# Kernel optimization log

Hardware: AMD Instinct MI355X
Metric: run time of the kernel (lower is better)

The kernel has to match this reference:

```python
import jax, jax.numpy as jnp
import numpy as np

EPS = 1e-3  # keras LayerNormalization default epsilon


def layer_norm(x, g, b):
    mu = jnp.mean(x, axis=-1, keepdims=True)
    var = jnp.mean(jnp.square(x - mu), axis=-1, keepdims=True)
    return g * (x - mu) / jnp.sqrt(var + EPS) + b


def setup_inputs() -> dict:
    key = jax.random.key(0)
    ks = jax.random.split(key, 16)
    B, S, E, H, F = 2, 4096, 512, 8, 2048
    s_e = 1.0 / np.sqrt(E)
    s_f = 1.0 / np.sqrt(F)
    inp = {
        "x": jax.random.normal(ks[0], (B, S, E), dtype=jnp.float32),
        "WQ": jax.random.normal(ks[1], (E, E), dtype=jnp.float32) * s_e,
        "bQ": jnp.zeros((E,), jnp.float32),
        "WK": jax.random.normal(ks[2], (E, E), dtype=jnp.float32) * s_e,
        "bK": jnp.zeros((E,), jnp.float32),
        "WV": jax.random.normal(ks[3], (E, E), dtype=jnp.float32) * s_e,
        "bV": jnp.zeros((E,), jnp.float32),
        "WO": jax.random.normal(ks[4], (E, E), dtype=jnp.float32) * s_e,
        "bO": jnp.zeros((E,), jnp.float32),
        "W1": jax.random.normal(ks[5], (E, F), dtype=jnp.float32) * s_e,
        "b1": jnp.zeros((F,), jnp.float32),
        "W2": jax.random.normal(ks[6], (F, E), dtype=jnp.float32) * s_f,
        "b2": jnp.zeros((E,), jnp.float32),
        "g1": jnp.ones((E,), jnp.float32),
        "beta1": jnp.zeros((E,), jnp.float32),
        "g2": jnp.ones((E,), jnp.float32),
        "beta2": jnp.zeros((E,), jnp.float32),
        "num_head": 8,
    }
    return inp


def reference(x, WQ, bQ, WK, bK, WV, bV, WO, bO, W1, b1, W2, b2,
              g1, beta1, g2, beta2, num_head):
    B, S, E = x.shape
    H = num_head
    d = E // H
    scale = jnp.sqrt(jnp.asarray(d, jnp.float32))

    q = (x @ WQ + bQ).reshape(B, S, H, d).transpose(0, 2, 1, 3)  # [B,H,S,d]
    k = (x @ WK + bK).reshape(B, S, H, d).transpose(0, 2, 1, 3)
    v = (x @ WV + bV).reshape(B, S, H, d).transpose(0, 2, 1, 3)

    score = jnp.einsum('bhqd,bhkd->bhqk', q, k) / scale  # O(S^2) materialized, as in source
    attn = jax.nn.softmax(score, axis=-1)
    zs = jnp.einsum('bhqk,bhkd->bhqd', attn, v)  # [B,H,S,d]

    # Faithful to source bug: reshape [B,H,S,d] -> [B,S,E] WITHOUT transposing back
    zs = zs.reshape(B, S, E)
    zs = zs @ WO + bO

    z = layer_norm(zs + x, g1, beta1)
    r = jax.nn.relu(z @ W1 + b1) @ W2 + b2
    r = layer_norm(r + z, g2, beta2)
    return r
```

## Files before the change

kernel.cpp:

```cpp
#include <hip/hip_runtime.h>
#include <hip/hip_bf16.h>

typedef unsigned short u16;
typedef __attribute__((ext_vector_type(8))) short bf16x8;
typedef __attribute__((ext_vector_type(4))) float f32x4;
typedef __attribute__((ext_vector_type(16))) float f32x16;

static constexpr int BB = 2;
static constexpr int SS = 4096;
static constexpr int EE = 512;
static constexpr int HH = 8;
static constexpr int DD = 64;
static constexpr int FF = 2048;
static constexpr int NR = BB * SS;
static constexpr int QS = 3 * EE;

#define QSCALE 0.18033688011112042f

__device__ __forceinline__ u16 f2bf(float f) {
  union { float f; unsigned u; } v; v.f = f;
  unsigned r = v.u + 0x7FFFu + ((v.u >> 16) & 1u);
  return (u16)(r >> 16);
}
__device__ __forceinline__ unsigned pack2(float a, float b) {
  return (unsigned)f2bf(a) | ((unsigned)f2bf(b) << 16);
}
__device__ __forceinline__ float bf2f_lo(unsigned u) {
  union { unsigned u; float f; } v; v.u = u << 16; return v.f;
}
__device__ __forceinline__ float bf2f_hi(unsigned u) {
  union { unsigned u; float f; } v; v.u = u & 0xffff0000u; return v.f;
}
__device__ __forceinline__ unsigned cvtpk(float lo, float hi) {
  unsigned r;
  asm("v_cvt_pk_bf16_f32 %0, %1, %2" : "=v"(r) : "v"(lo), "v"(hi));
  return r;
}
__device__ __forceinline__ void perm32swap(unsigned& a, unsigned& b) {
  asm("v_permlane32_swap_b32 %0, %1" : "+v"(a), "+v"(b));
}
__device__ __forceinline__ void gload_lds16(const u16* g, u16* l) {
  __builtin_amdgcn_global_load_lds(
      (const __attribute__((address_space(1))) unsigned*)g,
      (__attribute__((address_space(3))) unsigned*)l, 16, 0, 0);
}

struct TrJob { const float* W; u16* Wt; int K, N, k0, n0; };

__device__ __forceinline__ void transp_tile(const float* W, u16* Wt, int K,
                                            int N, int k0, int n0, int t) {
  __shared__ float T[64][65];
  const int tn = t & 63, tk = t >> 6;
#pragma unroll
  for (int i = 0; i < 16; ++i) {
    int kk = tk * 16 + i;
    T[kk][tn] = W[(size_t)(k0 + kk) * N + n0 + tn];
  }
  __syncthreads();
#pragma unroll
  for (int i = 0; i < 16; ++i) {
    int nn = tk * 16 + i;
    Wt[(size_t)(n0 + nn) * K + k0 + tn] = f2bf(T[tn][nn]);
  }
}

__global__ __launch_bounds__(256) void prep_all(
    const float* __restrict__ x, u16* __restrict__ xb,
    const float* __restrict__ WQ, const float* __restrict__ WK,
    const float* __restrict__ WV, const float* __restrict__ WO,
    const float* __restrict__ W1, const float* __restrict__ W2,
    u16* __restrict__ Wqkv_t, u16* __restrict__ WO_t, u16* __restrict__ W1_t,
    u16* __restrict__ W2_t, const float* __restrict__ bQ,
    const float* __restrict__ bK, const float* __restrict__ bV,
    float* __restrict__ bqkv) {
  const int bx = blockIdx.x;
  const int t = threadIdx.x;
  if (bx < 2048) {
    int i = (bx * 256 + t) * 8;
    float4 a = *(const float4*)(x + i);
    float4 b = *(const float4*)(x + i + 4);
    uint4 u;
    u.x = pack2(a.x, a.y); u.y = pack2(a.z, a.w);
    u.z = pack2(b.x, b.y); u.w = pack2(b.z, b.w);
    *(uint4*)(xb + i) = u;
    return;
  }
  int idx = bx - 2048;
  if (idx < 768) {
    TrJob j;
    if (idx < 256) {
      const float* srcs[4] = {WQ, WK, WV, WO};
      u16* dsts[4] = {Wqkv_t, Wqkv_t + 512 * 512, Wqkv_t + 1024 * 512, WO_t};
      int w = idx >> 6, l = idx & 63;
      j = {srcs[w], dsts[w], 512, 512, (l & 7) * 64, (l >> 3) * 64};
    } else if (idx < 512) {
      int l = idx - 256;
      j = {W1, W1_t, 512, 2048, (l & 7) * 64, (l >> 3) * 64};
    } else {
      int l = idx - 512;
      j = {W2, W2_t, 2048, 512, (l & 31) * 64, (l >> 5) * 64};
    }
    transp_tile(j.W, j.Wt, j.K, j.N, j.k0, j.n0, t);
    return;
  }
  for (int i = t; i < QS; i += 256)
    bqkv[i] = i < 512 ? bQ[i] : (i < 1024 ? bK[i - 512] : bV[i - 1024]);
}

__global__ __launch_bounds__(256) void transp_v(const u16* __restrict__ qkvb,
                                                u16* __restrict__ vt) {
  __shared__ u16 T[64][72];
  const int s0 = blockIdx.x * 64, c0 = blockIdx.y * 64, b = blockIdx.z;
  const int t = threadIdx.x;
#pragma unroll
  for (int i = 0; i < 2; ++i) {
    int idx = t + i * 256;
    int row = idx >> 3, c8 = idx & 7;
    *(uint4*)(&T[row][c8 * 8]) = *(const uint4*)(
        &qkvb[((size_t)b * SS + s0 + row) * QS + 1024 + c0 + c8 * 8]);
  }
  __syncthreads();
#pragma unroll
  for (int i = 0; i < 2; ++i) {
    int idx = t + i * 256;
    int c = idx >> 3, s8 = idx & 7;
    u16 tmp[8];
#pragma unroll
    for (int j = 0; j < 8; ++j) tmp[j] = T[s8 * 8 + j][c];
    *(uint4*)(&vt[((size_t)b * EE + c0 + c) * SS + s0 + s8 * 8]) =
        *(uint4*)tmp;
  }
}

template <int RELU, int OUT_BF16, int SCALEQ = 0>
__global__ __launch_bounds__(256) void gemm128(
    const u16* __restrict__ A, const u16* __restrict__ Bt,
    const float* __restrict__ bias, void* __restrict__ Cout,
    int M, int N, int K) {
  __shared__ __align__(16) u16 As[128 * 64];
  __shared__ __align__(16) u16 Bs[128 * 64];
  const int t = threadIdx.x;
  const int lane = t & 63, wid = t >> 6;
  const int lm = lane & 15, lg = lane >> 4;
  const int bm = blockIdx.x * 128, bn = blockIdx.y * 128;
  const int wr = (wid >> 1) * 64, wc = (wid & 1) * 64;
  const int sr = lane >> 3;
  const int scb = (lane & 7) ^ sr;

  f32x4 acc[4][4];
#pragma unroll
  for (int i = 0; i < 4; ++i)
#pragma unroll
    for (int j = 0; j < 4; ++j) acc[i][j] = (f32x4){0.f, 0.f, 0.f, 0.f};

  for (int kb = 0; kb < K; kb += 64) {
    __syncthreads();
#pragma unroll
    for (int i = 0; i < 4; ++i) {
      int rr = wid * 32 + i * 8 + sr;
      gload_lds16(A + (size_t)(bm + rr) * K + kb + scb * 8,
                  &As[(wid * 32 + i * 8) * 64]);
      gload_lds16(Bt + (size_t)(bn + rr) * K + kb + scb * 8,
                  &Bs[(wid * 32 + i * 8) * 64]);
    }
    __syncthreads();

#pragma unroll
    for (int c = 0; c < 2; ++c) {
      bf16x8 af[4], bfr[4];
#pragma unroll
      for (int i = 0; i < 4; ++i) {
        int ar = wr + i * 16 + lm;
        af[i] = *(const bf16x8*)(&As[ar * 64 + (((c * 4 + lg) ^ (ar & 7)) << 3)]);
        int br = wc + i * 16 + lm;
        bfr[i] = *(const bf16x8*)(&Bs[br * 64 + (((c * 4 + lg) ^ (br & 7)) << 3)]);
      }
#pragma unroll
      for (int i = 0; i < 4; ++i)
#pragma unroll
        for (int j = 0; j < 4; ++j)
          acc[i][j] = __builtin_amdgcn_mfma_f32_16x16x32_bf16(
              af[i], bfr[j], acc[i][j], 0, 0, 0);
    }
  }

  float bi[4];
#pragma unroll
  for (int j = 0; j < 4; ++j) bi[j] = bias[bn + wc + j * 16 + lm];

#pragma unroll
  for (int i = 0; i < 4; ++i) {
#pragma unroll
    for (int j = 0; j < 4; ++j) {
      int col = bn + wc + j * 16 + lm;
#pragma unroll
      for (int r = 0; r < 4; ++r) {
        int row = bm + wr + i * 16 + lg * 4 + r;
        float vv = acc[i][j][r] + bi[j];
        if (RELU) vv = fmaxf(vv, 0.f);
        if (SCALEQ && col < 512) vv *= QSCALE;
        if (OUT_BF16)
          ((u16*)Cout)[(size_t)row * N + col] = f2bf(vv);
        else
          ((float*)Cout)[(size_t)row * N + col] = vv;
      }
    }
  }
}

template <int RELU, int OUT_BF16, int SCALEQ = 0>
__global__ __launch_bounds__(256) void gemm64(
    const u16* __restrict__ A, const u16* __restrict__ Bt,
    const float* __restrict__ bias, void* __restrict__ Cout,
    int M, int N, int K) {
  __shared__ __align__(16) u16 As[2][64 * 64];
  __shared__ __align__(16) u16 Bs[2][64 * 64];
  const int t = threadIdx.x;
  const int lane = t & 63, wid = t >> 6;
  const int lm = lane & 15, lg = lane >> 4;
  const int bm = blockIdx.x * 64, bn = blockIdx.y * 64;
  const int wr = (wid >> 1) * 32, wc = (wid & 1) * 32;
  const int sr = lane >> 3;
  const int scb = (lane & 7) ^ sr;

  f32x4 acc[2][2];
#pragma unroll
  for (int i = 0; i < 2; ++i)
#pragma unroll
    for (int j = 0; j < 2; ++j) acc[i][j] = (f32x4){0.f, 0.f, 0.f, 0.f};

  auto stage = [&](int kb, int buf) {
#pragma unroll
    for (int i = 0; i < 2; ++i) {
      int r8 = wid * 16 + i * 8;
      gload_lds16(A + (size_t)(bm + r8 + sr) * K + kb + scb * 8,
                  &As[buf][r8 * 64]);
      gload_lds16(Bt + (size_t)(bn + r8 + sr) * K + kb + scb * 8,
                  &Bs[buf][r8 * 64]);
    }
  };

  stage(0, 0);
  const int nsteps = K >> 6;
  for (int s = 0; s < nsteps; ++s) {
    const int cur = s & 1;
    if (s + 1 < nsteps) {
      stage((s + 1) << 6, cur ^ 1);
      asm volatile("s_waitcnt vmcnt(4)" ::: "memory");
    } else {
      asm volatile("s_waitcnt vmcnt(0)" ::: "memory");
    }
    __builtin_amdgcn_sched_barrier(0);
    __builtin_amdgcn_s_barrier();

#pragma unroll
    for (int c = 0; c < 2; ++c) {
      bf16x8 af[2], bfr[2];
#pragma unroll
      for (int i = 0; i < 2; ++i) {
        int ar = wr + i * 16 + lm;
        af[i] = *(const bf16x8*)(
            &As[cur][ar * 64 + (((c * 4 + lg) ^ (ar & 7)) << 3)]);
        int br = wc + i * 16 + lm;
        bfr[i] = *(const bf16x8*)(
            &Bs[cur][br * 64 + (((c * 4 + lg) ^ (br & 7)) << 3)]);
      }
#pragma unroll
      for (int i = 0; i < 2; ++i)
#pragma unroll
        for (int j = 0; j < 2; ++j)
          acc[i][j] = __builtin_amdgcn_mfma_f32_16x16x32_bf16(
              af[i], bfr[j], acc[i][j], 0, 0, 0);
    }

    asm volatile("s_waitcnt lgkmcnt(0)" ::: "memory");
    __builtin_amdgcn_s_barrier();
  }

  float bi[2];
#pragma unroll
  for (int j = 0; j < 2; ++j) bi[j] = bias[bn + wc + j * 16 + lm];

#pragma unroll
  for (int i = 0; i < 2; ++i) {
#pragma unroll
    for (int j = 0; j < 2; ++j) {
      int col = bn + wc + j * 16 + lm;
#pragma unroll
      for (int r = 0; r < 4; ++r) {
        int row = bm + wr + i * 16 + lg * 4 + r;
        float vv = acc[i][j][r] + bi[j];
        if (RELU) vv = fmaxf(vv, 0.f);
        if (SCALEQ && col < 512) vv *= QSCALE;
        if (OUT_BF16)
          ((u16*)Cout)[(size_t)row * N + col] = f2bf(vv);
        else
          ((float*)Cout)[(size_t)row * N + col] = vv;
      }
    }
  }
}

__global__ __launch_bounds__(128, 4) void attn_split(
    const u16* __restrict__ qkv, const u16* __restrict__ vt,
    u16* __restrict__ po, float* __restrict__ pl) {
  __shared__ __align__(16) u16 K_lds[2][32 * 64];
  __shared__ __align__(16) u16 V_lds[2][64 * 32];

  const int bh = blockIdx.x;
  const int qblock = blockIdx.y;
  const int half = blockIdx.z;
  po += (size_t)half * (9u << 19);
  pl += (size_t)half * (1u << 18);
  const int b = bh >> 3, h = bh & 7;
  const int t = threadIdx.x;
  const int lane = t & 63, wid = t >> 6;
  const int q32 = lane & 31, hi = lane >> 5;
  const int qs7 = q32 & 7;
  const int vswz = (q32 & 3) ^ ((q32 >> 2) & 3);
  const size_t bS = (size_t)b * SS;
  const int koff0 = half * 2048;
  const u16* kp = qkv + 512;
  const u16* vrow = vt + ((size_t)b * EE + h * DD) * SS;
  const int qbase = qblock * 64 + wid * 32;

  bf16x8 qf[4];
  {
    const u16* qrow = qkv + (bS + qbase + q32) * QS + h * DD + hi * 8;
#pragma unroll
    for (int c = 0; c < 4; ++c) qf[c] = *(const bf16x8*)(qrow + c * 16);
  }
  bf16x8 onesf;
#pragma unroll
  for (int i = 0; i < 8; ++i) onesf[i] = (short)0x3F80;

  const int sr = lane >> 3;
  const int scb = (lane & 7) ^ sr;
  const int vr = lane >> 2;
  const int vcb = (lane & 3) ^ (vr & 3) ^ ((vr >> 2) & 3);

  f32x16 o0, o1, ol, z16;
#pragma unroll
  for (int i = 0; i < 16; ++i) {
    o0[i] = 0.f; o1[i] = 0.f; ol[i] = 0.f; z16[i] = 0.f;
  }

  auto stage = [&](int kt, int bufi) {
#pragma unroll
    for (int i = 0; i < 2; ++i) {
      int rb = wid * 16 + i * 8;
      gload_lds16(
          kp + (bS + koff0 + kt * 32 + rb + sr) * QS + h * DD + scb * 8,
          &K_lds[bufi][rb * 64]);
    }
#pragma unroll
    for (int i = 0; i < 2; ++i) {
      int rb = wid * 32 + i * 16;
      gload_lds16(vrow + (size_t)(rb + vr) * SS + koff0 + kt * 32 + vcb * 8,
                  &V_lds[bufi][rb * 32]);
    }
  };

  stage(0, 0);

  constexpr int NT = 2048 / 32;
  for (int kt = 0; kt < NT; ++kt) {
    const int cur = kt & 1;
    if (kt + 1 < NT) {
      stage(kt + 1, cur ^ 1);
      asm volatile("s_waitcnt vmcnt(4)" ::: "memory");
    } else {
      asm volatile("s_waitcnt vmcnt(0)" ::: "memory");
    }
    __builtin_amdgcn_sched_barrier(0);
    __builtin_amdgcn_s_barrier();

    f32x16 s;
    __builtin_amdgcn_s_setprio(1);
    {
      bf16x8 kf = *(const bf16x8*)(
          &K_lds[cur][q32 * 64 + ((hi ^ qs7) << 3)]);
      s = __builtin_amdgcn_mfma_f32_32x32x16_bf16(kf, qf[0], z16, 0, 0, 0);
    }
#pragma unroll
    for (int c = 1; c < 4; ++c) {
      bf16x8 kf = *(const bf16x8*)(
          &K_lds[cur][q32 * 64 + (((2 * c + hi) ^ qs7) << 3)]);
      s = __builtin_amdgcn_mfma_f32_32x32x16_bf16(kf, qf[c], s, 0, 0, 0);
    }
    __builtin_amdgcn_s_setprio(0);
    float p[16];
#pragma unroll
    for (int r = 0; r < 16; ++r) p[r] = __builtin_amdgcn_exp2f(s[r]);

    __builtin_amdgcn_s_setprio(1);
#pragma unroll
    for (int kc = 0; kc < 2; ++kc) {
      const int rA = kc * 8, rB = rA + 4;
      unsigned wA0 = cvtpk(p[rA + 0], p[rA + 1]);
      unsigned wA1 = cvtpk(p[rA + 2], p[rA + 3]);
      unsigned wB0 = cvtpk(p[rB + 0], p[rB + 1]);
      unsigned wB1 = cvtpk(p[rB + 2], p[rB + 3]);
      perm32swap(wA0, wB0);
      perm32swap(wA1, wB1);
      union { unsigned u[4]; bf16x8 v; } pf;
      pf.u[0] = wA0; pf.u[1] = wA1; pf.u[2] = wB0; pf.u[3] = wB1;
      bf16x8 vf0 = *(const bf16x8*)(
          &V_lds[cur][q32 * 32 + (((2 * kc + hi) ^ vswz) << 3)]);
      bf16x8 vf1 = *(const bf16x8*)(
          &V_lds[cur][(32 + q32) * 32 + (((2 * kc + hi) ^ vswz) << 3)]);
      o0 = __builtin_amdgcn_mfma_f32_32x32x16_bf16(pf.v, vf0, o0, 0, 0, 0);
      o1 = __builtin_amdgcn_mfma_f32_32x32x16_bf16(pf.v, vf1, o1, 0, 0, 0);
      ol = __builtin_amdgcn_mfma_f32_32x32x16_bf16(pf.v, onesf, ol, 0, 0, 0);
    }
    __builtin_amdgcn_s_setprio(0);

    asm volatile("s_waitcnt lgkmcnt(0)" ::: "memory");
    __builtin_amdgcn_s_barrier();
  }

  const size_t rowbase = (size_t)bh * 4096 + qbase;
#pragma unroll
  for (int reg = 0; reg < 16; ++reg) {
    int q = (reg & 3) + 8 * (reg >> 2) + 4 * hi;
    if (q32 == q) pl[rowbase + q] = ol[reg];
    u16* dst = po + (rowbase + q) * 64;
    dst[q32] = f2bf(o0[reg]);
    dst[32 + q32] = f2bf(o1[reg]);
  }
}

__global__ __launch_bounds__(256) void attn_combine(
    const u16* __restrict__ po0, const u16* __restrict__ po1,
    const float* __restrict__ pl0, const float* __restrict__ pl1,
    u16* __restrict__ zs) {
  const int row = blockIdx.x * 32 + (threadIdx.x >> 3);
  const int dblk = (threadIdx.x & 7) * 8;
  const int bh = row >> 12, s = row & 4095;
  const int b = bh >> 3, h = bh & 7;
  const float inv = 1.f / (pl0[row] + pl1[row]);
  uint4 a = *(const uint4*)(po0 + (size_t)row * 64 + dblk);
  uint4 c = *(const uint4*)(po1 + (size_t)row * 64 + dblk);
  uint4 r;
  r.x = pack2((bf2f_lo(a.x) + bf2f_lo(c.x)) * inv,
              (bf2f_hi(a.x) + bf2f_hi(c.x)) * inv);
  r.y = pack2((bf2f_lo(a.y) + bf2f_lo(c.y)) * inv,
              (bf2f_hi(a.y) + bf2f_hi(c.y)) * inv);
  r.z = pack2((bf2f_lo(a.z) + bf2f_lo(c.z)) * inv,
              (bf2f_hi(a.z) + bf2f_hi(c.z)) * inv);
  r.w = pack2((bf2f_lo(a.w) + bf2f_lo(c.w)) * inv,
              (bf2f_hi(a.w) + bf2f_hi(c.w)) * inv);
  u16* dst = zs + ((size_t)b * SS + h * 512 + (s >> 3)) * EE + (s & 7) * 64;
  *(uint4*)(dst + dblk) = r;
}

template <int WF32>
__global__ __launch_bounds__(128) void add_ln_b(
    const u16* __restrict__ a, const u16* __restrict__ xres,
    const float* __restrict__ g, const float* __restrict__ beta,
    u16* __restrict__ outb, float* __restrict__ outf) {
  const int row = blockIdx.x;
  const int tid = threadIdx.x;
  uint2 av = *(const uint2*)(a + (size_t)row * EE + tid * 4);
  uint2 xv = *(const uint2*)(xres + (size_t)row * EE + tid * 4);
  float vx = bf2f_lo(av.x) + bf2f_lo(xv.x);
  float vy = bf2f_hi(av.x) + bf2f_hi(xv.x);
  float vz = bf2f_lo(av.y) + bf2f_lo(xv.y);
  float vw = bf2f_hi(av.y) + bf2f_hi(xv.y);
  float sum = vx + vy + vz + vw;
  float sq = vx * vx + vy * vy + vz * vz + vw * vw;
#pragma unroll
  for (int off = 1; off < 64; off <<= 1) {
    sum += __shfl_xor(sum, off);
    sq += __shfl_xor(sq, off);
  }
  __shared__ float s0[2], s1[2];
  int w = tid >> 6;
  if ((tid & 63) == 0) { s0[w] = sum; s1[w] = sq; }
  __syncthreads();
  sum = s0[0] + s0[1];
  sq = s1[0] + s1[1];
  float mu = sum * (1.0f / EE);
  float var = sq * (1.0f / EE) - mu * mu;
  float r = rsqrtf(var + 1e-3f);
  int c = tid * 4;
  float4 gv = *(const float4*)(g + c);
  float4 bv = *(const float4*)(beta + c);
  float o0 = gv.x * (vx - mu) * r + bv.x;
  float o1 = gv.y * (vy - mu) * r + bv.y;
  float o2 = gv.z * (vz - mu) * r + bv.z;
  float o3 = gv.w * (vw - mu) * r + bv.w;
  if (WF32) {
    float4 ov = {o0, o1, o2, o3};
    *(float4*)(outf + (size_t)row * EE + c) = ov;
  } else {
    uint2 u;
    u.x = pack2(o0, o1);
    u.y = pack2(o2, o3);
    *(uint2*)(outb + (size_t)row * EE + c) = u;
  }
}

extern "C" void kernel_launch(void* const* d_in, const int* in_sizes, int n_in,
                              void* d_out, int out_size, void* d_ws,
                              size_t ws_size, hipStream_t stream) {
  const float* x = (const float*)d_in[0];
  const float* WQ = (const float*)d_in[1];
  const float* bQ = (const float*)d_in[2];
  const float* WK = (const float*)d_in[3];
  const float* bK = (const float*)d_in[4];
  const float* WV = (const float*)d_in[5];
  const float* bV = (const float*)d_in[6];
  const float* WO = (const float*)d_in[7];
  const float* bO = (const float*)d_in[8];
  const float* W1 = (const float*)d_in[9];
  const float* b1 = (const float*)d_in[10];
  const float* W2 = (const float*)d_in[11];
  const float* b2 = (const float*)d_in[12];
  const float* g1 = (const float*)d_in[13];
  const float* be1 = (const float*)d_in[14];
  const float* g2 = (const float*)d_in[15];
  const float* be2 = (const float*)d_in[16];
  float* out = (float*)d_out;

  const size_t MB = 1u << 20;
  char* w = (char*)d_ws;
  u16* Wqkv_t = (u16*)(w + 0);
  u16* WO_t   = (u16*)(w + 2 * MB);
  u16* W1_t   = (u16*)(w + 3 * MB);
  u16* W2_t   = (u16*)(w + 5 * MB);
  float* bqkv = (float*)(w + 7 * MB);
  u16* qkvb = (u16*)(w + 8 * MB);
  u16* zsb  = (u16*)(w + 32 * MB);
  u16* po0  = (u16*)(w + 40 * MB);
  u16* po1  = (u16*)(w + 49 * MB);
  float* pl0 = (float*)(w + 58 * MB);
  float* pl1 = (float*)(w + 59 * MB);
  u16* zs2b = (u16*)(w + 40 * MB);
  u16* f2b  = (u16*)(w + 49 * MB);
  u16* zb   = (u16*)(w + 72 * MB);
  u16* xb   = (u16*)(w + 80 * MB);
  u16* vtb  = (u16*)(w + 88 * MB);
  u16* f1   = (u16*)(w + 8 * MB);

  dim3 blk(256);

  prep_all<<<dim3(2817), blk, 0, stream>>>(x, xb, WQ, WK, WV, WO, W1, W2,
                                           Wqkv_t, WO_t, W1_t, W2_t, bQ, bK,
                                           bV, bqkv);
  gemm128<0, 1, 1><<<dim3(64, 12), blk, 0, stream>>>(xb, Wqkv_t, bqkv, qkvb,
                                                     NR, QS, EE);
  transp_v<<<dim3(SS / 64, EE / 64, BB), blk, 0, stream>>>(qkvb, vtb);
  attn_split<<<dim3(BB * HH, SS / 64, 2), dim3(128), 0, stream>>>(qkvb, vtb,
                                                                  po0, pl0);
  attn_combine<<<dim3(2048), blk, 0, stream>>>(po0, po1, pl0, pl1, zsb);
  gemm64<0, 1><<<dim3(128, 8), blk, 0, stream>>>(zsb, WO_t, bO, zs2b,
                                                 NR, EE, EE);
  add_ln_b<0><<<dim3(NR), dim3(128), 0, stream>>>(zs2b, xb, g1, be1, zb,
                                                  nullptr);
  gemm128<1, 1><<<dim3(64, 16), blk, 0, stream>>>(zb, W1_t, b1, f1,
                                                  NR, FF, EE);
  gemm64<0, 1><<<dim3(128, 8), blk, 0, stream>>>(f1, W2_t, b2, f2b,
                                                 NR, EE, FF);
  add_ln_b<1><<<dim3(NR), dim3(128), 0, stream>>>(f2b, zb, g2, be2, nullptr,
                                                  out);
}
```

Measured before the change: 219.8 us.

## Fuse split-K attention halves into one block and combine in LDS

The two key-halves of attention now run as separate wave pairs inside one 256-thread block rather than as separate blocks, and their partial outputs are combined through LDS. This removes the separate combine kernel and the global round trip of partial outputs and row sums. It also replaces the ones-matrix MFMA used for the row sum with a scalar accumulation of the exponentials. In exchange, blocks are larger and need more LDS, and the epilogue adds a barrier and LDS traffic.

```diff
diff --git a/kernel.cpp b/kernel.cpp
--- a/kernel.cpp
+++ b/kernel.cpp
@@ -301,20 +301,17 @@
   }
 }
 
-__global__ __launch_bounds__(128, 4) void attn_split(
+__global__ __launch_bounds__(256, 4) void attn_fused(
     const u16* __restrict__ qkv, const u16* __restrict__ vt,
-    u16* __restrict__ po, float* __restrict__ pl) {
-  __shared__ __align__(16) u16 K_lds[2][32 * 64];
-  __shared__ __align__(16) u16 V_lds[2][64 * 32];
+    u16* __restrict__ zs) {
+  __shared__ __align__(16) u16 KV[2][2][4096];
 
   const int bh = blockIdx.x;
   const int qblock = blockIdx.y;
-  const int half = blockIdx.z;
-  po += (size_t)half * (9u << 19);
-  pl += (size_t)half * (1u << 18);
   const int b = bh >> 3, h = bh & 7;
   const int t = threadIdx.x;
   const int lane = t & 63, wid = t >> 6;
+  const int qsub = wid & 1, half = wid >> 1;
   const int q32 = lane & 31, hi = lane >> 5;
   const int qs7 = q32 & 7;
   const int vswz = (q32 & 3) ^ ((q32 >> 2) & 3);
@@ -322,7 +319,7 @@
   const int koff0 = half * 2048;
   const u16* kp = qkv + 512;
   const u16* vrow = vt + ((size_t)b * EE + h * DD) * SS;
-  const int qbase = qblock * 64 + wid * 32;
+  const int qbase = qblock * 64 + qsub * 32;
 
   bf16x8 qf[4];
   {
@@ -330,34 +327,30 @@
 #pragma unroll
     for (int c = 0; c < 4; ++c) qf[c] = *(const bf16x8*)(qrow + c * 16);
   }
-  bf16x8 onesf;
-#pragma unroll
-  for (int i = 0; i < 8; ++i) onesf[i] = (short)0x3F80;
 
   const int sr = lane >> 3;
   const int scb = (lane & 7) ^ sr;
   const int vr = lane >> 2;
   const int vcb = (lane & 3) ^ (vr & 3) ^ ((vr >> 2) & 3);
 
-  f32x16 o0, o1, ol, z16;
-#pragma unroll
-  for (int i = 0; i < 16; ++i) {
-    o0[i] = 0.f; o1[i] = 0.f; ol[i] = 0.f; z16[i] = 0.f;
-  }
+  f32x16 o0, o1, z16;
+#pragma unroll
+  for (int i = 0; i < 16; ++i) { o0[i] = 0.f; o1[i] = 0.f; z16[i] = 0.f; }
+  float lsum = 0.f;
 
   auto stage = [&](int kt, int bufi) {
 #pragma unroll
     for (int i = 0; i < 2; ++i) {
-      int rb = wid * 16 + i * 8;
+      int rb = qsub * 16 + i * 8;
       gload_lds16(
           kp + (bS + koff0 + kt * 32 + rb + sr) * QS + h * DD + scb * 8,
-          &K_lds[bufi][rb * 64]);
+          &KV[bufi][half][rb * 64]);
     }
 #pragma unroll
     for (int i = 0; i < 2; ++i) {
-      int rb = wid * 32 + i * 16;
+      int rb = qsub * 32 + i * 16;
       gload_lds16(vrow + (size_t)(rb + vr) * SS + koff0 + kt * 32 + vcb * 8,
-                  &V_lds[bufi][rb * 32]);
+                  &KV[bufi][half][2048 + rb * 32]);
     }
   };
 
@@ -375,23 +368,28 @@
     __builtin_amdgcn_sched_barrier(0);
     __builtin_amdgcn_s_barrier();
 
+    const u16* Kl = &KV[cur][half][0];
+    const u16* Vl = &KV[cur][half][2048];
+
     f32x16 s;
     __builtin_amdgcn_s_setprio(1);
     {
-      bf16x8 kf = *(const bf16x8*)(
-          &K_lds[cur][q32 * 64 + ((hi ^ qs7) << 3)]);
+      bf16x8 kf = *(const bf16x8*)(&Kl[q32 * 64 + ((hi ^ qs7) << 3)]);
       s = __builtin_amdgcn_mfma_f32_32x32x16_bf16(kf, qf[0], z16, 0, 0, 0);
     }
 #pragma unroll
     for (int c = 1; c < 4; ++c) {
       bf16x8 kf = *(const bf16x8*)(
-          &K_lds[cur][q32 * 64 + (((2 * c + hi) ^ qs7) << 3)]);
+          &Kl[q32 * 64 + (((2 * c + hi) ^ qs7) << 3)]);
       s = __builtin_amdgcn_mfma_f32_32x32x16_bf16(kf, qf[c], s, 0, 0, 0);
     }
     __builtin_amdgcn_s_setprio(0);
     float p[16];
 #pragma unroll
-    for (int r = 0; r < 16; ++r) p[r] = __builtin_amdgcn_exp2f(s[r]);
+    for (int r = 0; r < 16; ++r) {
+      p[r] = __builtin_amdgcn_exp2f(s[r]);
+      lsum += p[r];
+    }
 
     __builtin_amdgcn_s_setprio(1);
 #pragma unroll
@@ -406,12 +404,11 @@
       union { unsigned u[4]; bf16x8 v; } pf;
       pf.u[0] = wA0; pf.u[1] = wA1; pf.u[2] = wB0; pf.u[3] = wB1;
       bf16x8 vf0 = *(const bf16x8*)(
-          &V_lds[cur][q32 * 32 + (((2 * kc + hi) ^ vswz) << 3)]);
+          &Vl[q32 * 32 + (((2 * kc + hi) ^ vswz) << 3)]);
       bf16x8 vf1 = *(const bf16x8*)(
-          &V_lds[cur][(32 + q32) * 32 + (((2 * kc + hi) ^ vswz) << 3)]);
+          &Vl[(32 + q32) * 32 + (((2 * kc + hi) ^ vswz) << 3)]);
       o0 = __builtin_amdgcn_mfma_f32_32x32x16_bf16(pf.v, vf0, o0, 0, 0, 0);
       o1 = __builtin_amdgcn_mfma_f32_32x32x16_bf16(pf.v, vf1, o1, 0, 0, 0);
-      ol = __builtin_amdgcn_mfma_f32_32x32x16_bf16(pf.v, onesf, ol, 0, 0, 0);
     }
     __builtin_amdgcn_s_setprio(0);
 
@@ -419,39 +416,35 @@
     __builtin_amdgcn_s_barrier();
   }
 
-  const size_t rowbase = (size_t)bh * 4096 + qbase;
-#pragma unroll
-  for (int reg = 0; reg < 16; ++reg) {
-    int q = (reg & 3) + 8 * (reg >> 2) + 4 * hi;
-    if (q32 == q) pl[rowbase + q] = ol[reg];
-    u16* dst = po + (rowbase + q) * 64;
-    dst[q32] = f2bf(o0[reg]);
-    dst[32 + q32] = f2bf(o1[reg]);
-  }
-}
-
-__global__ __launch_bounds__(256) void attn_combine(
-    const u16* __restrict__ po0, const u16* __restrict__ po1,
-    const float* __restrict__ pl0, const float* __restrict__ pl1,
-    u16* __restrict__ zs) {
-  const int row = blockIdx.x * 32 + (threadIdx.x >> 3);
-  const int dblk = (threadIdx.x & 7) * 8;
-  const int bh = row >> 12, s = row & 4095;
-  const int b = bh >> 3, h = bh & 7;
-  const float inv = 1.f / (pl0[row] + pl1[row]);
-  uint4 a = *(const uint4*)(po0 + (size_t)row * 64 + dblk);
-  uint4 c = *(const uint4*)(po1 + (size_t)row * 64 + dblk);
-  uint4 r;
-  r.x = pack2((bf2f_lo(a.x) + bf2f_lo(c.x)) * inv,
-              (bf2f_hi(a.x) + bf2f_hi(c.x)) * inv);
-  r.y = pack2((bf2f_lo(a.y) + bf2f_lo(c.y)) * inv,
-              (bf2f_hi(a.y) + bf2f_hi(c.y)) * inv);
-  r.z = pack2((bf2f_lo(a.z) + bf2f_lo(c.z)) * inv,
-              (bf2f_hi(a.z) + bf2f_hi(c.z)) * inv);
-  r.w = pack2((bf2f_lo(a.w) + bf2f_lo(c.w)) * inv,
-              (bf2f_hi(a.w) + bf2f_hi(c.w)) * inv);
-  u16* dst = zs + ((size_t)b * SS + h * 512 + (s >> 3)) * EE + (s & 7) * 64;
-  *(uint4*)(dst + dblk) = r;
+  float fl = lsum + __shfl_xor(lsum, 32);
+  float* ExO = (float*)&KV[0][0][0];
+  float* ExL = (float*)&KV[1][0][0];
+  if (lane < 32) ExL[(half * 2 + qsub) * 32 + q32] = fl;
+  if (half == 1) {
+#pragma unroll
+    for (int reg = 0; reg < 16; ++reg) {
+      int q = (reg & 3) + 8 * (reg >> 2) + 4 * hi;
+      ExO[(qsub * 32 + q) * 64 + q32] = o0[reg];
+      ExO[(qsub * 32 + q) * 64 + 32 + q32] = o1[reg];
+    }
+  }
+  asm volatile("s_waitcnt lgkmcnt(0)" ::: "memory");
+  __builtin_amdgcn_s_barrier();
+  if (half == 0) {
+#pragma unroll
+    for (int reg = 0; reg < 16; ++reg) {
+      int q = (reg & 3) + 8 * (reg >> 2) + 4 * hi;
+      float lt = ExL[qsub * 32 + q] + ExL[(2 + qsub) * 32 + q];
+      float inv = 1.f / lt;
+      float a0 = (o0[reg] + ExO[(qsub * 32 + q) * 64 + q32]) * inv;
+      float a1 = (o1[reg] + ExO[(qsub * 32 + q) * 64 + 32 + q32]) * inv;
+      int sq = qbase + q;
+      u16* dst =
+          zs + ((size_t)b * SS + h * 512 + (sq >> 3)) * EE + (sq & 7) * 64;
+      dst[q32] = f2bf(a0);
+      dst[32 + q32] = f2bf(a1);
+    }
+  }
 }
 
 template <int WF32>
@@ -532,12 +525,8 @@
   float* bqkv = (float*)(w + 7 * MB);
   u16* qkvb = (u16*)(w + 8 * MB);
   u16* zsb  = (u16*)(w + 32 * MB);
-  u16* po0  = (u16*)(w + 40 * MB);
-  u16* po1  = (u16*)(w + 49 * MB);
-  float* pl0 = (float*)(w + 58 * MB);
-  float* pl1 = (float*)(w + 59 * MB);
   u16* zs2b = (u16*)(w + 40 * MB);
-  u16* f2b  = (u16*)(w + 49 * MB);
+  u16* f2b  = (u16*)(w + 48 * MB);
   u16* zb   = (u16*)(w + 72 * MB);
   u16* xb   = (u16*)(w + 80 * MB);
   u16* vtb  = (u16*)(w + 88 * MB);
@@ -551,9 +540,7 @@
   gemm128<0, 1, 1><<<dim3(64, 12), blk, 0, stream>>>(xb, Wqkv_t, bqkv, qkvb,
                                                      NR, QS, EE);
   transp_v<<<dim3(SS / 64, EE / 64, BB), blk, 0, stream>>>(qkvb, vtb);
-  attn_split<<<dim3(BB * HH, SS / 64, 2), dim3(128), 0, stream>>>(qkvb, vtb,
-                                                                  po0, pl0);
-  attn_combine<<<dim3(2048), blk, 0, stream>>>(po0, po1, pl0, pl1, zsb);
+  attn_fused<<<dim3(BB * HH, SS / 64), blk, 0, stream>>>(qkvb, vtb, zsb);
   gemm64<0, 1><<<dim3(128, 8), blk, 0, stream>>>(zsb, WO_t, bO, zs2b,
                                                  NR, EE, EE);
   add_ln_b<0><<<dim3(NR), dim3(128), 0, stream>>>(zs2b, xb, g1, be1, zb,
```

Result: faster. 211.7 us (-3.7%).
